# Kernel tuning notes

Measured on AMD Instinct MI355X. Metric: run time of the kernel, lower is better.

## Reference

```python
import jax, jax.numpy as jnp
from jax import lax
import numpy as np

V, E, H, B, S = 50000, 512, 256, 32, 1024  # H = hidden_dim // 2 per direction


def _lstm(x, W_ih, W_hh, b_ih, b_hh, lengths):
    """Batch-first unidirectional LSTM; outputs zeroed beyond per-sample length
    (matches pack_padded_sequence -> pad_packed_sequence semantics for outputs).
    x: (B, S, E); W_ih: (4H, E); W_hh: (4H, H). Gate order i, f, g, o (PyTorch).
    """
    b, s, _ = x.shape
    h_dim = W_hh.shape[1]
    # precompute input projections for all timesteps: (S, B, 4H)
    xg = jnp.einsum('bse,ge->sbg', x, W_ih) + b_ih + b_hh

    def step(carry, xt):
        h, c = carry
        gates = xt + h @ W_hh.T
        i, f, g, o = jnp.split(gates, 4, axis=-1)
        c = jax.nn.sigmoid(f) * c + jax.nn.sigmoid(i) * jnp.tanh(g)
        h = jax.nn.sigmoid(o) * jnp.tanh(c)
        return (h, c), h

    init = (jnp.zeros((b, h_dim), x.dtype), jnp.zeros((b, h_dim), x.dtype))
    _, hs = lax.scan(step, init, xg)
    hs = jnp.swapaxes(hs, 0, 1)  # (B, S, H)
    tmask = jnp.arange(s)[None, :] < lengths[:, None]
    return hs * tmask[:, :, None].astype(hs.dtype)


def setup_inputs() -> dict:
    key = jax.random.key(0)
    ks = jax.random.split(key, 12)
    inputs = jax.random.randint(ks[0], (B, S), 0, V)
    lengths = jnp.sort(jax.random.randint(ks[1], (B,), S // 2, S + 1))[::-1]
    lengths = lengths.at[0].set(S)  # pad_packed returns max length
    t = jnp.arange(S)[None, :]
    in_len = (t < lengths[:, None]).astype(jnp.int32)
    fmask = jax.random.randint(ks[2], (B, S), 0, 2).astype(jnp.int32) * in_len
    bmask = jax.random.randint(ks[3], (B, S), 0, 2).astype(jnp.int32) * in_len
    emb_scale = np.sqrt(3.0 / E)
    emb = jax.random.uniform(ks[4], (V, E), jnp.float32, -emb_scale, emb_scale)
    k = 1.0 / np.sqrt(H)
    u = lambda kk, shp: jax.random.uniform(kk, shp, jnp.float32, -k, k)
    return {
        'inputs': inputs, 'seq_length': lengths, 'fmask': fmask, 'bmask': bmask,
        'out_seq_length': S,
        'emb': emb,
        'f_Wih': u(ks[5], (4 * H, E)), 'f_Whh': u(ks[6], (4 * H, H)),
        'f_bih': u(ks[7], (4 * H,)), 'f_bhh': jnp.zeros((4 * H,), jnp.float32),
        'b_Wih': u(ks[8], (4 * H, E)), 'b_Whh': u(ks[9], (4 * H, H)),
        'b_bih': u(ks[10], (4 * H,)), 'b_bhh': jnp.zeros((4 * H,), jnp.float32),
    }


def reference(inputs, seq_length, fmask, bmask, out_seq_length,
              emb, f_Wih, f_Whh, f_bih, f_bhh, b_Wih, b_Whh, b_bih, b_bhh):
    b, s = inputs.shape
    pos = jnp.arange(s)
    mb = fmask.astype(bool)
    # stable argsort puts masked (True) positions first, preserving order
    order = jnp.argsort(~mb, axis=1)  # (B, S)
    counts = mb.sum(axis=1)  # (B,)
    valid = (pos[None, :] < counts[:, None])  # (B, S)

    # forward direction (dropout p=0.0 -> identity)
    x = emb[inputs]
    f_out = _lstm(x, f_Wih, f_Whh, f_bih, f_bhh, seq_length)  # (B, S, H)
    f_comp = jnp.take_along_axis(f_out, order[:, :, None], axis=1)
    f_comp = f_comp * valid[:, :, None].astype(f_comp.dtype)

    # backward direction: reverse each row within its length, pad token 0
    t = pos[None, :]
    in_len = t < seq_length[:, None]
    rev_t = jnp.where(in_len, seq_length[:, None] - 1 - t, 0)
    rev_inputs = jnp.where(in_len, jnp.take_along_axis(inputs, rev_t, axis=1), 0)
    xb = emb[rev_inputs]
    b_out = _lstm(xb, b_Wih, b_Whh, b_bih, b_bhh, seq_length)  # (B, S, H)
    # NOTE: original code selects b_lstm_out with fmask (not bmask) — faithful
    b_comp = jnp.take_along_axis(b_out, order[:, :, None], axis=1)
    b_comp = b_comp * valid[:, :, None].astype(b_comp.dtype)
    # reverse the compacted selection within its count
    rev_j = jnp.clip(counts[:, None] - 1 - pos[None, :], 0, s - 1)
    b_rev = jnp.take_along_axis(b_comp, rev_j[:, :, None], axis=1)
    b_rev = b_rev * valid[:, :, None].astype(b_rev.dtype)

    out = jnp.concatenate([f_comp, b_rev], axis=2)  # (B, S, 2H)
    return out[:, :out_seq_length]
```

## Files before the change

kernel.cpp:

```cpp
#include <hip/hip_runtime.h>

#define VV 50000
#define EE 512
#define HH 256
#define BB 32
#define SS 1024
#define G4 1024

typedef __attribute__((ext_vector_type(8))) short short8;
typedef __attribute__((ext_vector_type(4))) float float4v;
typedef __attribute__((ext_vector_type(2))) float float2v;
typedef __attribute__((ext_vector_type(4))) unsigned short ushort4v;
typedef __attribute__((ext_vector_type(4))) unsigned int uint4v;

#define MFMA(a, b, c) __builtin_amdgcn_mfma_f32_16x16x32_bf16(a, b, c, 0, 0, 0)

__device__ __forceinline__ float b2f(unsigned short u) {
  union { unsigned int i; float f; } v; v.i = ((unsigned int)u) << 16; return v.f;
}
__device__ __forceinline__ unsigned short f2b(float f) {
  union { float f; unsigned int i; } v; v.f = f;
  unsigned int u = v.i;
  return (unsigned short)((u + 0x7fffu + ((u >> 16) & 1u)) >> 16);
}
__device__ __forceinline__ short8 pack8(const float* p) {
  float4v x0 = *(const float4v*)p;
  float4v x1 = *(const float4v*)(p + 4);
  short8 r;
  r[0] = (short)f2b(x0[0]); r[1] = (short)f2b(x0[1]);
  r[2] = (short)f2b(x0[2]); r[3] = (short)f2b(x0[3]);
  r[4] = (short)f2b(x1[0]); r[5] = (short)f2b(x1[1]);
  r[6] = (short)f2b(x1[2]); r[7] = (short)f2b(x1[3]);
  return r;
}
__device__ __forceinline__ float sigm(float x) {
  return __builtin_amdgcn_rcpf(1.0f + __expf(-x));
}
__device__ __forceinline__ float tanh_f(float x) {
  return 1.0f - 2.0f * __builtin_amdgcn_rcpf(__expf(2.0f * x) + 1.0f);
}

__global__ __launch_bounds__(256) void k_scan(const int* __restrict__ fmask,
                                              int* __restrict__ order,
                                              int* __restrict__ counts) {
  __shared__ int sh[256];
  const int b = blockIdx.x;
  const int tid = threadIdx.x;
  int m0[4];
  const int base = b * SS + tid * 4;
#pragma unroll
  for (int j = 0; j < 4; ++j) m0[j] = fmask[base + j];
  const int s = m0[0] + m0[1] + m0[2] + m0[3];
  sh[tid] = s;
  __syncthreads();
  for (int off = 1; off < 256; off <<= 1) {
    int v = 0;
    if (tid >= off) v = sh[tid - off];
    __syncthreads();
    sh[tid] += v;
    __syncthreads();
  }
  const int incl = sh[tid];
  int pos = incl - s;
#pragma unroll
  for (int j = 0; j < 4; ++j) {
    if (m0[j]) order[b * SS + pos++] = tid * 4 + j;
  }
  if (tid == 255) counts[b] = incl;
}

#define BM 128
#define BN 128
#define BK 32
#define LSTR 56

__global__ __launch_bounds__(256, 2) void k_gemm(
    const int* __restrict__ inputs, const int* __restrict__ seqlen,
    const float* __restrict__ emb,
    const float* __restrict__ Wih_f, const float* __restrict__ Wih_b,
    const float* __restrict__ bih_f, const float* __restrict__ bih_b,
    const float* __restrict__ bhh_f, const float* __restrict__ bhh_b,
    unsigned short* __restrict__ xg) {
  __shared__ short As[BM * LSTR];
  __shared__ short Bs[BN * LSTR];
  __shared__ int tokL[BM];

  const int d = blockIdx.y;
  const int mt = blockIdx.x >> 3, nt = blockIdx.x & 7;
  const int Mbase = mt * BM, Nbase = nt * BN;
  const int tid = threadIdx.x;
  const float* Wih = d ? Wih_b : Wih_f;

  if (tid < BM) {
    const int m = Mbase + tid;
    const int t = m >> 5, b = m & 31;
    int tok;
    if (d == 0) {
      tok = inputs[b * SS + t];
    } else {
      const int L = seqlen[b];
      tok = (t < L) ? inputs[b * SS + (L - 1 - t)] : 0;
    }
    tokL[tid] = tok;
  }
  __syncthreads();

  const int wave = tid >> 6, lane = tid & 63, ln = lane & 15, q = lane >> 4;
  const int wm = wave & 1, wn = wave >> 1;

  float4v acc[4][4];
#pragma unroll
  for (int ni = 0; ni < 4; ++ni)
#pragma unroll
    for (int mi = 0; mi < 4; ++mi) acc[ni][mi] = (float4v){0.f, 0.f, 0.f, 0.f};

  for (int kb = 0; kb < (EE / BK); ++kb) {
    const int k0 = kb * BK;
    if (kb) __syncthreads();
#pragma unroll
    for (int i = 0; i < 2; ++i) {
      const int c = tid + i * 256;
      const int row = c >> 2, sub = c & 3;
      const short8 av = pack8(emb + (size_t)tokL[row] * EE + k0 + sub * 8);
      *(short8*)(As + row * LSTR + sub * 8) = av;
      const short8 bv = pack8(Wih + (size_t)(Nbase + row) * EE + k0 + sub * 8);
      *(short8*)(Bs + row * LSTR + sub * 8) = bv;
    }
    __syncthreads();
    short8 af[4], bfr[4];
#pragma unroll
    for (int mi = 0; mi < 4; ++mi)
      af[mi] = *(const short8*)(As + (wm * 64 + mi * 16 + ln) * LSTR + q * 8);
#pragma unroll
    for (int ni = 0; ni < 4; ++ni)
      bfr[ni] = *(const short8*)(Bs + (wn * 64 + ni * 16 + ln) * LSTR + q * 8);
#pragma unroll
    for (int ni = 0; ni < 4; ++ni)
#pragma unroll
      for (int mi = 0; mi < 4; ++mi)
        acc[ni][mi] = MFMA(bfr[ni], af[mi], acc[ni][mi]);
  }

  const float* bih = d ? bih_b : bih_f;
  const float* bhh = d ? bhh_b : bhh_f;
  float biasv[4][4];
#pragma unroll
  for (int ni = 0; ni < 4; ++ni)
#pragma unroll
    for (int r = 0; r < 4; ++r) {
      const int col = Nbase + wn * 64 + ni * 16 + q * 4 + r;
      biasv[ni][r] = bih[col] + bhh[col];
    }
#pragma unroll
  for (int ni = 0; ni < 4; ++ni) {
    const int gate0 = Nbase + wn * 64 + ni * 16 + q * 4;
#pragma unroll
    for (int mi = 0; mi < 4; ++mi) {
      const int m = Mbase + wm * 64 + mi * 16 + ln;
      const int t = m >> 5, b0 = m & 31;
      ushort4v pk;
#pragma unroll
      for (int r = 0; r < 4; ++r) pk[r] = f2b(acc[ni][mi][r] + biasv[ni][r]);
      *(ushort4v*)(xg + (((size_t)d * SS + t) * BB + b0) * G4 + gate0) = pk;
    }
  }
}

#define SENTQ 0x7f7f7f7f7f7f7f7full
#define PMAGIC 0x51A600

__device__ __forceinline__ int l2probe(const int* p) {
  int v;
  asm volatile("global_load_dword %0, %1, off sc0 nt\n\t"
               "s_waitcnt vmcnt(0)"
               : "=v"(v) : "v"(p) : "memory");
  return v;
}

__device__ __forceinline__ void l2row8(const void* p, uint4v* r) {
  asm volatile(
      "global_load_dwordx4 %0, %8, off sc0 nt\n\t"
      "global_load_dwordx4 %1, %8, off offset:64 sc0 nt\n\t"
      "global_load_dwordx4 %2, %8, off offset:128 sc0 nt\n\t"
      "global_load_dwordx4 %3, %8, off offset:192 sc0 nt\n\t"
      "global_load_dwordx4 %4, %8, off offset:256 sc0 nt\n\t"
      "global_load_dwordx4 %5, %8, off offset:320 sc0 nt\n\t"
      "global_load_dwordx4 %6, %8, off offset:384 sc0 nt\n\t"
      "global_load_dwordx4 %7, %8, off offset:448 sc0 nt\n\t"
      "s_waitcnt vmcnt(0)"
      : "=&v"(r[0]), "=&v"(r[1]), "=&v"(r[2]), "=&v"(r[3]),
        "=&v"(r[4]), "=&v"(r[5]), "=&v"(r[6]), "=&v"(r[7])
      : "v"(p)
      : "memory");
}

__global__ __launch_bounds__(256, 1) void k_recur(
    const float* __restrict__ Whh_f, const float* __restrict__ Whh_b,
    const unsigned short* __restrict__ xg, unsigned short* __restrict__ hbuf,
    int* __restrict__ proto) {
  __shared__ unsigned long long lbuf[2][BB][8];
  __shared__ int s_mode;

  const int beta = blockIdx.x;
  const int xcd = beta & 7, slot = beta >> 3;
  if (xcd >= 2) return;
  const int d = xcd, k = slot;
  const float* Whh = d ? Whh_b : Whh_f;
  const int tid = threadIdx.x;
  const int lane = tid & 63, ln = lane & 15, q = lane >> 4;
  const int wave = tid >> 6;
  const int g = wave & 1, nw = wave >> 1;
  const int chain = nw * 16 + ln;
  const int ubase = k * 32 + g * 16 + q * 4;
  const int lqw = g * 4 + q;

  if (tid == 0) {
    int* probes = proto;
    int* vote_ok = proto + 16;
    int* vote_n = proto + 18;
    probes[d * 8 + k] = PMAGIC + k;
    int ok = 0;
    for (int it = 0; it < 256 && !ok; ++it) {
      ok = 1;
#pragma unroll
      for (int s = 0; s < 8; ++s)
        ok &= (l2probe(probes + d * 8 + s) == PMAGIC + s);
    }
    __hip_atomic_fetch_add(vote_ok + d, ok, __ATOMIC_RELAXED,
                           __HIP_MEMORY_SCOPE_AGENT);
    __hip_atomic_fetch_add(vote_n + d, 1, __ATOMIC_RELEASE,
                           __HIP_MEMORY_SCOPE_AGENT);
    while (__hip_atomic_load(vote_n + d, __ATOMIC_ACQUIRE,
                             __HIP_MEMORY_SCOPE_AGENT) < 8) {}
    s_mode = (__hip_atomic_load(vote_ok + d, __ATOMIC_RELAXED,
                                __HIP_MEMORY_SCOPE_AGENT) == 8);
  }
  __syncthreads();
  const int mode_l2 = s_mode;

  short8 w[4][8];
#pragma unroll
  for (int G = 0; G < 4; ++G) {
    const int grow = G * 256 + k * 32 + g * 16 + ln;
#pragma unroll
    for (int kt = 0; kt < 8; ++kt)
      w[G][kt] = pack8(Whh + (size_t)grow * HH + kt * 32 + q * 8);
  }

  float c4[4] = {0.f, 0.f, 0.f, 0.f};
  unsigned short* hb = hbuf + (size_t)d * 1025 * BB * HH;
  const unsigned short* xgd = xg + (size_t)d * SS * BB * G4;

  ushort4v xc4[4], xn4[4];
#pragma unroll
  for (int G = 0; G < 4; ++G)
    xc4[G] = *(const ushort4v*)(xgd + ((size_t)0 * BB + chain) * G4 + G * 256 + ubase);

  if (mode_l2) {
    for (int t = 0; t < SS; ++t) {
      if (t + 1 < SS) {
#pragma unroll
        for (int G = 0; G < 4; ++G)
          xn4[G] = *(const ushort4v*)(xgd + ((size_t)(t + 1) * BB + chain) * G4 +
                                      G * 256 + ubase);
      }

      float4v acc[4];
#pragma unroll
      for (int G = 0; G < 4; ++G) acc[G] = (float4v){0.f, 0.f, 0.f, 0.f};

      if (t > 0) {
        union Q16 { uint4v v; unsigned long long qq[2]; short8 s8; } rr[8];
        const char* hq =
            (const char*)(hb + ((size_t)t * BB + chain) * HH) + q * 16;
        for (;;) {
          uint4v tmp[8];
          l2row8(hq, tmp);
#pragma unroll
          for (int j = 0; j < 8; ++j) rr[j].v = tmp[j];
          bool bad = false;
#pragma unroll
          for (int j = 0; j < 8; ++j)
            bad |= (rr[j].qq[0] == SENTQ) | (rr[j].qq[1] == SENTQ);
          if (!bad) break;
        }
#pragma unroll
        for (int kt = 0; kt < 8; ++kt)
#pragma unroll
          for (int G = 0; G < 4; ++G) acc[G] = MFMA(w[G][kt], rr[kt].s8, acc[G]);
      }

      unsigned long long pv = 0ull;
#pragma unroll
      for (int r = 0; r < 4; ++r) {
        const float gi = acc[0][r] + b2f(xc4[0][r]);
        const float gf = acc[1][r] + b2f(xc4[1][r]);
        const float gg = acc[2][r] + b2f(xc4[2][r]);
        const float go = acc[3][r] + b2f(xc4[3][r]);
        const float cn = sigm(gf) * c4[r] + sigm(gi) * tanh_f(gg);
        c4[r] = cn;
        const float h = sigm(go) * tanh_f(cn);
        pv |= ((unsigned long long)f2b(h)) << (16 * r);
      }
      *(unsigned long long*)(hb + ((size_t)(t + 1) * BB + chain) * HH + ubase) = pv;

#pragma unroll
      for (int G = 0; G < 4; ++G) xc4[G] = xn4[G];
    }
  } else {
    for (int t = 0; t < SS; ++t) {
      if (t + 1 < SS) {
#pragma unroll
        for (int G = 0; G < 4; ++G)
          xn4[G] = *(const ushort4v*)(xgd + ((size_t)(t + 1) * BB + chain) * G4 +
                                      G * 256 + ubase);
      }

      unsigned long long qv[16];
      if (t > 0) {
        const unsigned long long own0 = lbuf[t & 1][chain][2 * q];
        const unsigned long long own1 = lbuf[t & 1][chain][2 * q + 1];
        const unsigned long long* hq =
            (const unsigned long long*)(hb + ((size_t)t * BB + chain) * HH) + q * 2;
        for (;;) {
#pragma unroll
          for (int i = 0; i < 16; ++i)
            qv[i] = __hip_atomic_load(hq + (i >> 1) * 8 + (i & 1),
                                      __ATOMIC_RELAXED, __HIP_MEMORY_SCOPE_AGENT);
#pragma unroll
          for (int i = 0; i < 16; ++i)
            if ((i >> 1) == k) qv[i] = (i & 1) ? own1 : own0;
          bool bad = false;
#pragma unroll
          for (int i = 0; i < 16; ++i) bad |= (qv[i] == SENTQ);
          if (!bad) break;
          __builtin_amdgcn_s_sleep(1);
        }
      }

      float4v acc[4];
#pragma unroll
      for (int G = 0; G < 4; ++G) acc[G] = (float4v){0.f, 0.f, 0.f, 0.f};
      if (t > 0) {
#pragma unroll
        for (int kt = 0; kt < 8; ++kt) {
          union { unsigned long long u[2]; short8 s; } hh;
          hh.u[0] = qv[kt * 2]; hh.u[1] = qv[kt * 2 + 1];
#pragma unroll
          for (int G = 0; G < 4; ++G) acc[G] = MFMA(w[G][kt], hh.s, acc[G]);
        }
      }

      unsigned long long pv = 0ull;
#pragma unroll
      for (int r = 0; r < 4; ++r) {
        const float gi = acc[0][r] + b2f(xc4[0][r]);
        const float gf = acc[1][r] + b2f(xc4[1][r]);
        const float gg = acc[2][r] + b2f(xc4[2][r]);
        const float go = acc[3][r] + b2f(xc4[3][r]);
        const float cn = sigm(gf) * c4[r] + sigm(gi) * tanh_f(gg);
        c4[r] = cn;
        const float h = sigm(go) * tanh_f(cn);
        pv |= ((unsigned long long)f2b(h)) << (16 * r);
      }
      __hip_atomic_store(
          (unsigned long long*)(hb + ((size_t)(t + 1) * BB + chain) * HH + ubase),
          pv, __ATOMIC_RELAXED, __HIP_MEMORY_SCOPE_AGENT);
      lbuf[(t + 1) & 1][chain][lqw] = pv;

      __builtin_amdgcn_sched_barrier(0);
      asm volatile("s_waitcnt lgkmcnt(0)" ::: "memory");
      __builtin_amdgcn_s_barrier();
      __builtin_amdgcn_sched_barrier(0);

#pragma unroll
      for (int G = 0; G < 4; ++G) xc4[G] = xn4[G];
    }
  }
}

__global__ __launch_bounds__(256) void k_gather(
    const unsigned short* __restrict__ hbuf, const int* __restrict__ order,
    const int* __restrict__ counts, float* __restrict__ out) {
  const int bj = blockIdx.x;
  const int b = bj >> 10, j = bj & 1023;
  const int tid = threadIdx.x;
  const int cnt = counts[b];
  float2v val = (float2v){0.f, 0.f};
  if (j < cnt) {
    const int half = tid >> 7;
    const int e2 = (tid & 127) * 2;
    const int tsel = half ? order[b * SS + (cnt - 1 - j)] : order[b * SS + j];
    const unsigned short* src =
        hbuf + (((size_t)half * 1025 + (tsel + 1)) * BB + b) * HH + e2;
    const unsigned int u = *(const unsigned int*)src;
    val[0] = b2f((unsigned short)u);
    val[1] = b2f((unsigned short)(u >> 16));
  }
  *(float2v*)(out + (size_t)bj * 512 + tid * 2) = val;
}

extern "C" void kernel_launch(void* const* d_in, const int* in_sizes, int n_in,
                              void* d_out, int out_size, void* d_ws, size_t ws_size,
                              hipStream_t stream) {
  (void)in_sizes; (void)n_in; (void)out_size; (void)ws_size;
  const int* inputs = (const int*)d_in[0];
  const int* seqlen = (const int*)d_in[1];
  const int* fmask  = (const int*)d_in[2];
  const float* emb  = (const float*)d_in[5];
  const float* fWih = (const float*)d_in[6];
  const float* fWhh = (const float*)d_in[7];
  const float* fbih = (const float*)d_in[8];
  const float* fbhh = (const float*)d_in[9];
  const float* bWih = (const float*)d_in[10];
  const float* bWhh = (const float*)d_in[11];
  const float* bbih = (const float*)d_in[12];
  const float* bbhh = (const float*)d_in[13];
  float* out = (float*)d_out;

  char* ws = (char*)d_ws;
  int* proto  = (int*)(ws + 0);
  int* counts = (int*)(ws + 12800);
  int* order  = (int*)(ws + 16384);
  const size_t o_hbuf = (size_t)1 << 18;
  unsigned short* hbuf = (unsigned short*)(ws + o_hbuf);
  const size_t hbuf_bytes = (size_t)2 * 1025 * BB * HH * 2;
  const size_t o_xg = o_hbuf + hbuf_bytes;
  unsigned short* xg = (unsigned short*)(ws + o_xg);

  hipMemsetAsync(proto, 0, 128, stream);
  hipMemsetAsync(hbuf, 0x7f, hbuf_bytes, stream);

  k_scan<<<32, 256, 0, stream>>>(fmask, order, counts);
  k_gemm<<<dim3(2048, 2), 256, 0, stream>>>(inputs, seqlen, emb, fWih, bWih,
                                            fbih, bbih, fbhh, bbhh, xg);
  k_recur<<<64, 256, 0, stream>>>(fWhh, bWhh, xg, hbuf, proto);
  k_gather<<<BB * SS, 256, 0, stream>>>(hbuf, order, counts, out);
}
```

Before: 2.849 ms.

## Split recurrence across two 512-thread blocks per direction with LDS half-sharing

The LSTM recurrence moves from eight 256-thread blocks per direction to two 512-thread blocks per direction. Each block computes 128 hidden units for all 32 chains. The block's own half of h comes from swizzled LDS, and only the peer block's half is polled through L2. MFMAs on the local half are issued while the remote loads are in flight, and the time loop is unrolled by two to ping-pong the prefetched input-gate buffers. This is meant to cut cross-block global traffic and the width of the spin-wait synchronisation per step. In exchange, each block carries more MFMA work and registers per step, and fewer CUs are used.

```diff
diff --git a/kernel.cpp b/kernel.cpp
--- a/kernel.cpp
+++ b/kernel.cpp
@@ -177,63 +177,80 @@
   return v;
 }
 
-__device__ __forceinline__ void l2row8(const void* p, uint4v* r) {
+__device__ __forceinline__ void l2pair_issue(const void* p0, const void* p1,
+                                             uint4v* r) {
   asm volatile(
       "global_load_dwordx4 %0, %8, off sc0 nt\n\t"
       "global_load_dwordx4 %1, %8, off offset:64 sc0 nt\n\t"
       "global_load_dwordx4 %2, %8, off offset:128 sc0 nt\n\t"
       "global_load_dwordx4 %3, %8, off offset:192 sc0 nt\n\t"
-      "global_load_dwordx4 %4, %8, off offset:256 sc0 nt\n\t"
-      "global_load_dwordx4 %5, %8, off offset:320 sc0 nt\n\t"
-      "global_load_dwordx4 %6, %8, off offset:384 sc0 nt\n\t"
-      "global_load_dwordx4 %7, %8, off offset:448 sc0 nt\n\t"
+      "global_load_dwordx4 %4, %9, off sc0 nt\n\t"
+      "global_load_dwordx4 %5, %9, off offset:64 sc0 nt\n\t"
+      "global_load_dwordx4 %6, %9, off offset:128 sc0 nt\n\t"
+      "global_load_dwordx4 %7, %9, off offset:192 sc0 nt\n\t"
+      : "=&v"(r[0]), "=&v"(r[1]), "=&v"(r[2]), "=&v"(r[3]),
+        "=&v"(r[4]), "=&v"(r[5]), "=&v"(r[6]), "=&v"(r[7])
+      : "v"(p0), "v"(p1)
+      : "memory");
+}
+__device__ __forceinline__ void l2pair(const void* p0, const void* p1,
+                                       uint4v* r) {
+  asm volatile(
+      "global_load_dwordx4 %0, %8, off sc0 nt\n\t"
+      "global_load_dwordx4 %1, %8, off offset:64 sc0 nt\n\t"
+      "global_load_dwordx4 %2, %8, off offset:128 sc0 nt\n\t"
+      "global_load_dwordx4 %3, %8, off offset:192 sc0 nt\n\t"
+      "global_load_dwordx4 %4, %9, off sc0 nt\n\t"
+      "global_load_dwordx4 %5, %9, off offset:64 sc0 nt\n\t"
+      "global_load_dwordx4 %6, %9, off offset:128 sc0 nt\n\t"
+      "global_load_dwordx4 %7, %9, off offset:192 sc0 nt\n\t"
       "s_waitcnt vmcnt(0)"
       : "=&v"(r[0]), "=&v"(r[1]), "=&v"(r[2]), "=&v"(r[3]),
         "=&v"(r[4]), "=&v"(r[5]), "=&v"(r[6]), "=&v"(r[7])
-      : "v"(p)
+      : "v"(p0), "v"(p1)
       : "memory");
 }
-
-__global__ __launch_bounds__(256, 1) void k_recur(
+__device__ __forceinline__ void vwait8(uint4v* r) {
+  asm volatile("s_waitcnt vmcnt(0)"
+               : "+v"(r[0]), "+v"(r[1]), "+v"(r[2]), "+v"(r[3]),
+                 "+v"(r[4]), "+v"(r[5]), "+v"(r[6]), "+v"(r[7])
+               :: "memory");
+}
+
+__global__ __launch_bounds__(512, 2) void k_recur(
     const float* __restrict__ Whh_f, const float* __restrict__ Whh_b,
     const unsigned short* __restrict__ xg, unsigned short* __restrict__ hbuf,
     int* __restrict__ proto) {
-  __shared__ unsigned long long lbuf[2][BB][8];
+  __shared__ unsigned short lh[2][BB][128];
   __shared__ int s_mode;
 
   const int beta = blockIdx.x;
-  const int xcd = beta & 7, slot = beta >> 3;
+  const int xcd = beta & 7, j = beta >> 3;
   if (xcd >= 2) return;
-  const int d = xcd, k = slot;
+  const int d = xcd;
   const float* Whh = d ? Whh_b : Whh_f;
   const int tid = threadIdx.x;
   const int lane = tid & 63, ln = lane & 15, q = lane >> 4;
-  const int wave = tid >> 6;
-  const int g = wave & 1, nw = wave >> 1;
-  const int chain = nw * 16 + ln;
-  const int ubase = k * 32 + g * 16 + q * 4;
-  const int lqw = g * 4 + q;
+  const int wv = tid >> 6;
 
   if (tid == 0) {
     int* probes = proto;
-    int* vote_ok = proto + 16;
-    int* vote_n = proto + 18;
-    probes[d * 8 + k] = PMAGIC + k;
+    int* vote_ok = proto + 8;
+    int* vote_n = proto + 10;
+    probes[d * 2 + j] = PMAGIC + d * 2 + j;
     int ok = 0;
-    for (int it = 0; it < 256 && !ok; ++it) {
-      ok = 1;
-#pragma unroll
-      for (int s = 0; s < 8; ++s)
-        ok &= (l2probe(probes + d * 8 + s) == PMAGIC + s);
+    for (int it = 0; it < 512 && !ok; ++it) {
+      ok = (l2probe(probes + d * 2 + 0) == PMAGIC + d * 2 + 0) &
+           (l2probe(probes + d * 2 + 1) == PMAGIC + d * 2 + 1);
     }
     __hip_atomic_fetch_add(vote_ok + d, ok, __ATOMIC_RELAXED,
                            __HIP_MEMORY_SCOPE_AGENT);
     __hip_atomic_fetch_add(vote_n + d, 1, __ATOMIC_RELEASE,
                            __HIP_MEMORY_SCOPE_AGENT);
     while (__hip_atomic_load(vote_n + d, __ATOMIC_ACQUIRE,
-                             __HIP_MEMORY_SCOPE_AGENT) < 8) {}
+                             __HIP_MEMORY_SCOPE_AGENT) < 2) {}
     s_mode = (__hip_atomic_load(vote_ok + d, __ATOMIC_RELAXED,
-                                __HIP_MEMORY_SCOPE_AGENT) == 8);
+                                __HIP_MEMORY_SCOPE_AGENT) == 2);
   }
   __syncthreads();
   const int mode_l2 = s_mode;
@@ -241,142 +258,201 @@
   short8 w[4][8];
 #pragma unroll
   for (int G = 0; G < 4; ++G) {
-    const int grow = G * 256 + k * 32 + g * 16 + ln;
-#pragma unroll
-    for (int kt = 0; kt < 8; ++kt)
-      w[G][kt] = pack8(Whh + (size_t)grow * HH + kt * 32 + q * 8);
-  }
-
-  float c4[4] = {0.f, 0.f, 0.f, 0.f};
+    const int grow = G * 256 + j * 128 + wv * 16 + ln;
+#pragma unroll
+    for (int i = 0; i < 8; ++i) {
+      const int kt_g = i ^ (j << 2);
+      w[G][i] = pack8(Whh + (size_t)grow * HH + kt_g * 32 + q * 8);
+    }
+  }
+
+  float c4[2][4] = {{0.f, 0.f, 0.f, 0.f}, {0.f, 0.f, 0.f, 0.f}};
   unsigned short* hb = hbuf + (size_t)d * 1025 * BB * HH;
   const unsigned short* xgd = xg + (size_t)d * SS * BB * G4;
-
-  ushort4v xc4[4], xn4[4];
+  const int uoff = j * 128 + wv * 16 + q * 4;
+  const int foff = (1 - j) * 128 + q * 8;
+  const int lws = ((wv * 16 + q * 4) * 2) ^ ((ln & 7) << 4);
+
+  ushort4v xga[4][2], xgb[4][2];
 #pragma unroll
   for (int G = 0; G < 4; ++G)
-    xc4[G] = *(const ushort4v*)(xgd + ((size_t)0 * BB + chain) * G4 + G * 256 + ubase);
+#pragma unroll
+    for (int ct = 0; ct < 2; ++ct)
+      xga[G][ct] = *(const ushort4v*)(xgd + ((size_t)0 * BB + ct * 16 + ln) * G4 +
+                                      G * 256 + uoff);
+
+#define STEP_FAST(T_, XC, XN)                                                  \
+  {                                                                            \
+    const int t_ = (T_);                                                       \
+    float4v acc[4][2];                                                         \
+    _Pragma("unroll") for (int G = 0; G < 4; ++G)                              \
+        _Pragma("unroll") for (int ct = 0; ct < 2; ++ct)                       \
+            acc[G][ct] = (float4v){0.f, 0.f, 0.f, 0.f};                        \
+    uint4v f_[8];                                                              \
+    const unsigned short* fb0 = hb + ((size_t)t_ * BB + ln) * HH + foff;       \
+    const unsigned short* fb1 = hb + ((size_t)t_ * BB + 16 + ln) * HH + foff;  \
+    if (t_ > 0) {                                                              \
+      l2pair_issue(fb0, fb1, f_);         \
+      _Pragma("unroll") for (int ct = 0; ct < 2; ++ct) {                       \
+        const char* rb = (const char*)&lh[t_ & 1][ct * 16 + ln][0];            \
+        _Pragma("unroll") for (int ktl = 0; ktl < 4; ++ktl) {                  \
+          const int rs = (ktl * 64 + q * 16) ^ ((ln & 7) << 4);                \
+          const short8 fr = *(const short8*)(rb + rs);                         \
+          _Pragma("unroll") for (int G = 0; G < 4; ++G)                        \
+              acc[G][ct] = MFMA(w[G][ktl], fr, acc[G][ct]);                    \
+        }                                                                      \
+      }                                                                        \
+      vwait8(f_);                                                              \
+      __builtin_amdgcn_sched_barrier(0);                                       \
+      for (;;) {                                                               \
+        bool bad = false;                                                      \
+        _Pragma("unroll") for (int i = 0; i < 8; ++i) {                        \
+          union { uint4v v; unsigned long long qq[2]; } u;                     \
+          u.v = f_[i];                                                         \
+          bad |= (u.qq[0] == SENTQ) | (u.qq[1] == SENTQ);                      \
+        }                                                                      \
+        if (!bad) break;                                                       \
+        l2pair(fb0, fb1, f_);                                                  \
+        __builtin_amdgcn_sched_barrier(0);                                     \
+      }                                                                        \
+      _Pragma("unroll") for (int ktl = 0; ktl < 4; ++ktl) {                    \
+        union { uint4v v; short8 s8; } u0, u1;                                 \
+        u0.v = f_[ktl]; u1.v = f_[4 + ktl];                                    \
+        _Pragma("unroll") for (int G = 0; G < 4; ++G) {                        \
+          acc[G][0] = MFMA(w[G][4 + ktl], u0.s8, acc[G][0]);                   \
+          acc[G][1] = MFMA(w[G][4 + ktl], u1.s8, acc[G][1]);                   \
+        }                                                                      \
+      }                                                                        \
+    }                                                                          \
+    if (t_ + 1 < SS) {        \
+      _Pragma("unroll") for (int G = 0; G < 4; ++G)                            \
+          _Pragma("unroll") for (int ct = 0; ct < 2; ++ct)                     \
+              XN[G][ct] = *(const ushort4v*)(xgd +                             \
+                  ((size_t)(t_ + 1) * BB + ct * 16 + ln) * G4 + G * 256 +      \
+                  uoff);                                                       \
+    }                                                                          \
+    _Pragma("unroll") for (int ct = 0; ct < 2; ++ct) {                         \
+      unsigned long long pv = 0ull;                                            \
+      _Pragma("unroll") for (int r = 0; r < 4; ++r) {                          \
+        const float gi = acc[0][ct][r] + b2f(XC[0][ct][r]);                    \
+        const float gf = acc[1][ct][r] + b2f(XC[1][ct][r]);                    \
+        const float gg = acc[2][ct][r] + b2f(XC[2][ct][r]);                    \
+        const float go = acc[3][ct][r] + b2f(XC[3][ct][r]);                    \
+        const float cn = sigm(gf) * c4[ct][r] + sigm(gi) * tanh_f(gg);         \
+        c4[ct][r] = cn;                                                        \
+        const float h = sigm(go) * tanh_f(cn);                                 \
+        pv |= ((unsigned long long)f2b(h)) << (16 * r);                        \
+      }                                                                        \
+      *(unsigned long long*)(hb + ((size_t)(t_ + 1) * BB + ct * 16 + ln) * HH +\
+                             uoff) = pv;      \
+      *(unsigned long long*)((char*)&lh[(t_ + 1) & 1][ct * 16 + ln][0] +       \
+                             lws) = pv;                                        \
+    }                                                                          \
+    __builtin_amdgcn_sched_barrier(0);                                         \
+    asm volatile("s_waitcnt lgkmcnt(0)" ::: "memory");                         \
+    __builtin_amdgcn_s_barrier();                                              \
+    __builtin_amdgcn_sched_barrier(0);                                         \
+  }
 
   if (mode_l2) {
+    for (int t0 = 0; t0 < SS; t0 += 2) {
+      STEP_FAST(t0, xga, xgb);
+      STEP_FAST(t0 + 1, xgb, xga);
+    }
+  } else {
+    ushort4v xc[4][2], xn[4][2];
+#pragma unroll
+    for (int G = 0; G < 4; ++G)
+#pragma unroll
+      for (int ct = 0; ct < 2; ++ct) xc[G][ct] = xga[G][ct];
     for (int t = 0; t < SS; ++t) {
       if (t + 1 < SS) {
 #pragma unroll
         for (int G = 0; G < 4; ++G)
-          xn4[G] = *(const ushort4v*)(xgd + ((size_t)(t + 1) * BB + chain) * G4 +
-                                      G * 256 + ubase);
+#pragma unroll
+          for (int ct = 0; ct < 2; ++ct)
+            xn[G][ct] = *(const ushort4v*)(xgd +
+                ((size_t)(t + 1) * BB + ct * 16 + ln) * G4 + G * 256 + uoff);
       }
-
-      float4v acc[4];
-#pragma unroll
-      for (int G = 0; G < 4; ++G) acc[G] = (float4v){0.f, 0.f, 0.f, 0.f};
-
+      float4v acc[4][2];
+#pragma unroll
+      for (int G = 0; G < 4; ++G)
+#pragma unroll
+        for (int ct = 0; ct < 2; ++ct) acc[G][ct] = (float4v){0.f, 0.f, 0.f, 0.f};
       if (t > 0) {
-        union Q16 { uint4v v; unsigned long long qq[2]; short8 s8; } rr[8];
-        const char* hq =
-            (const char*)(hb + ((size_t)t * BB + chain) * HH) + q * 16;
+#pragma unroll
+        for (int ct = 0; ct < 2; ++ct) {
+          const char* rb = (const char*)&lh[t & 1][ct * 16 + ln][0];
+#pragma unroll
+          for (int ktl = 0; ktl < 4; ++ktl) {
+            const int rs = (ktl * 64 + q * 16) ^ ((ln & 7) << 4);
+            const short8 fr = *(const short8*)(rb + rs);
+#pragma unroll
+            for (int G = 0; G < 4; ++G) acc[G][ct] = MFMA(w[G][ktl], fr, acc[G][ct]);
+          }
+        }
+        unsigned long long fq0[8], fq1[8];
+        const unsigned long long* b0 =
+            (const unsigned long long*)(hb + ((size_t)t * BB + ln) * HH + foff);
+        const unsigned long long* b1 =
+            (const unsigned long long*)(hb + ((size_t)t * BB + 16 + ln) * HH + foff);
         for (;;) {
-          uint4v tmp[8];
-          l2row8(hq, tmp);
-#pragma unroll
-          for (int j = 0; j < 8; ++j) rr[j].v = tmp[j];
+#pragma unroll
+          for (int i = 0; i < 8; ++i) {
+            fq0[i] = __hip_atomic_load(b0 + (i >> 1) * 8 + (i & 1),
+                                       __ATOMIC_RELAXED, __HIP_MEMORY_SCOPE_AGENT);
+            fq1[i] = __hip_atomic_load(b1 + (i >> 1) * 8 + (i & 1),
+                                       __ATOMIC_RELAXED, __HIP_MEMORY_SCOPE_AGENT);
+          }
           bool bad = false;
 #pragma unroll
-          for (int j = 0; j < 8; ++j)
-            bad |= (rr[j].qq[0] == SENTQ) | (rr[j].qq[1] == SENTQ);
-          if (!bad) break;
-        }
-#pragma unroll
-        for (int kt = 0; kt < 8; ++kt)
-#pragma unroll
-          for (int G = 0; G < 4; ++G) acc[G] = MFMA(w[G][kt], rr[kt].s8, acc[G]);
-      }
-
-      unsigned long long pv = 0ull;
-#pragma unroll
-      for (int r = 0; r < 4; ++r) {
-        const float gi = acc[0][r] + b2f(xc4[0][r]);
-        const float gf = acc[1][r] + b2f(xc4[1][r]);
-        const float gg = acc[2][r] + b2f(xc4[2][r]);
-        const float go = acc[3][r] + b2f(xc4[3][r]);
-        const float cn = sigm(gf) * c4[r] + sigm(gi) * tanh_f(gg);
-        c4[r] = cn;
-        const float h = sigm(go) * tanh_f(cn);
-        pv |= ((unsigned long long)f2b(h)) << (16 * r);
-      }
-      *(unsigned long long*)(hb + ((size_t)(t + 1) * BB + chain) * HH + ubase) = pv;
-
-#pragma unroll
-      for (int G = 0; G < 4; ++G) xc4[G] = xn4[G];
-    }
-  } else {
-    for (int t = 0; t < SS; ++t) {
-      if (t + 1 < SS) {
-#pragma unroll
-        for (int G = 0; G < 4; ++G)
-          xn4[G] = *(const ushort4v*)(xgd + ((size_t)(t + 1) * BB + chain) * G4 +
-                                      G * 256 + ubase);
-      }
-
-      unsigned long long qv[16];
-      if (t > 0) {
-        const unsigned long long own0 = lbuf[t & 1][chain][2 * q];
-        const unsigned long long own1 = lbuf[t & 1][chain][2 * q + 1];
-        const unsigned long long* hq =
-            (const unsigned long long*)(hb + ((size_t)t * BB + chain) * HH) + q * 2;
-        for (;;) {
-#pragma unroll
-          for (int i = 0; i < 16; ++i)
-            qv[i] = __hip_atomic_load(hq + (i >> 1) * 8 + (i & 1),
-                                      __ATOMIC_RELAXED, __HIP_MEMORY_SCOPE_AGENT);
-#pragma unroll
-          for (int i = 0; i < 16; ++i)
-            if ((i >> 1) == k) qv[i] = (i & 1) ? own1 : own0;
-          bool bad = false;
-#pragma unroll
-          for (int i = 0; i < 16; ++i) bad |= (qv[i] == SENTQ);
+          for (int i = 0; i < 8; ++i) bad |= (fq0[i] == SENTQ) | (fq1[i] == SENTQ);
           if (!bad) break;
           __builtin_amdgcn_s_sleep(1);
         }
-      }
-
-      float4v acc[4];
-#pragma unroll
-      for (int G = 0; G < 4; ++G) acc[G] = (float4v){0.f, 0.f, 0.f, 0.f};
-      if (t > 0) {
-#pragma unroll
-        for (int kt = 0; kt < 8; ++kt) {
-          union { unsigned long long u[2]; short8 s; } hh;
-          hh.u[0] = qv[kt * 2]; hh.u[1] = qv[kt * 2 + 1];
-#pragma unroll
-          for (int G = 0; G < 4; ++G) acc[G] = MFMA(w[G][kt], hh.s, acc[G]);
+#pragma unroll
+        for (int ktl = 0; ktl < 4; ++ktl) {
+          union { unsigned long long u[2]; short8 s; } h0, h1;
+          h0.u[0] = fq0[ktl * 2]; h0.u[1] = fq0[ktl * 2 + 1];
+          h1.u[0] = fq1[ktl * 2]; h1.u[1] = fq1[ktl * 2 + 1];
+#pragma unroll
+          for (int G = 0; G < 4; ++G) {
+            acc[G][0] = MFMA(w[G][4 + ktl], h0.s, acc[G][0]);
+            acc[G][1] = MFMA(w[G][4 + ktl], h1.s, acc[G][1]);
+          }
         }
       }
-
-      unsigned long long pv = 0ull;
-#pragma unroll
-      for (int r = 0; r < 4; ++r) {
-        const float gi = acc[0][r] + b2f(xc4[0][r]);
-        const float gf = acc[1][r] + b2f(xc4[1][r]);
-        const float gg = acc[2][r] + b2f(xc4[2][r]);
-        const float go = acc[3][r] + b2f(xc4[3][r]);
-        const float cn = sigm(gf) * c4[r] + sigm(gi) * tanh_f(gg);
-        c4[r] = cn;
-        const float h = sigm(go) * tanh_f(cn);
-        pv |= ((unsigned long long)f2b(h)) << (16 * r);
+#pragma unroll
+      for (int ct = 0; ct < 2; ++ct) {
+        unsigned long long pv = 0ull;
+#pragma unroll
+        for (int r = 0; r < 4; ++r) {
+          const float gi = acc[0][ct][r] + b2f(xc[0][ct][r]);
+          const float gf = acc[1][ct][r] + b2f(xc[1][ct][r]);
+          const float gg = acc[2][ct][r] + b2f(xc[2][ct][r]);
+          const float go = acc[3][ct][r] + b2f(xc[3][ct][r]);
+          const float cn = sigm(gf) * c4[ct][r] + sigm(gi) * tanh_f(gg);
+          c4[ct][r] = cn;
+          const float h = sigm(go) * tanh_f(cn);
+          pv |= ((unsigned long long)f2b(h)) << (16 * r);
+        }
+        __hip_atomic_store(
+            (unsigned long long*)(hb + ((size_t)(t + 1) * BB + ct * 16 + ln) * HH +
+                                  uoff),
+            pv, __ATOMIC_RELAXED, __HIP_MEMORY_SCOPE_AGENT);
+        *(unsigned long long*)((char*)&lh[(t + 1) & 1][ct * 16 + ln][0] + lws) = pv;
       }
-      __hip_atomic_store(
-          (unsigned long long*)(hb + ((size_t)(t + 1) * BB + chain) * HH + ubase),
-          pv, __ATOMIC_RELAXED, __HIP_MEMORY_SCOPE_AGENT);
-      lbuf[(t + 1) & 1][chain][lqw] = pv;
-
       __builtin_amdgcn_sched_barrier(0);
       asm volatile("s_waitcnt lgkmcnt(0)" ::: "memory");
       __builtin_amdgcn_s_barrier();
       __builtin_amdgcn_sched_barrier(0);
-
-#pragma unroll
-      for (int G = 0; G < 4; ++G) xc4[G] = xn4[G];
-    }
-  }
+#pragma unroll
+      for (int G = 0; G < 4; ++G)
+#pragma unroll
+        for (int ct = 0; ct < 2; ++ct) xc[G][ct] = xn[G][ct];
+    }
+  }
+#undef STEP_FAST
 }
 
 __global__ __launch_bounds__(256) void k_gather(
@@ -434,6 +510,6 @@
   k_scan<<<32, 256, 0, stream>>>(fmask, order, counts);
   k_gemm<<<dim3(2048, 2), 256, 0, stream>>>(inputs, seqlen, emb, fWih, bWih,
                                             fbih, bbih, fbhh, bbhh, xg);
-  k_recur<<<64, 256, 0, stream>>>(fWhh, bWhh, xg, hbuf, proto);
+  k_recur<<<16, 512, 0, stream>>>(fWhh, bWhh, xg, hbuf, proto);
   k_gather<<<BB * SS, 256, 0, stream>>>(hbuf, order, counts, out);
 }
```

After: 7.154 ms. 2.51x slower.
